# Kernel tuning notes

Hardware: AMD Instinct MI355X
Metric: run time of the kernel (lower is better)

## Reference

```python
import jax, jax.numpy as jnp
import numpy as np
import math

B, N, D = 4, 1024, 1024
H = 16
HD = D // H          # 64
TOP_K = 64
NUM_STATIC = 32


def setup_inputs() -> dict:
    key = jax.random.key(0)
    ks = jax.random.split(key, 10)
    s = 1.0 / math.sqrt(D)  # ~ nn.Linear default init scale
    inp = {
        "x": jax.random.normal(ks[0], (B, N, D), dtype=jnp.float32),
        "Wq": jax.random.uniform(ks[1], (D, D), jnp.float32, -s, s),
        "bq": jax.random.uniform(ks[2], (D,), jnp.float32, -s, s),
        "Wk": jax.random.uniform(ks[3], (D, D), jnp.float32, -s, s),
        "bk": jax.random.uniform(ks[4], (D,), jnp.float32, -s, s),
        "Wv": jax.random.uniform(ks[5], (D, D), jnp.float32, -s, s),
        "bv": jax.random.uniform(ks[6], (D,), jnp.float32, -s, s),
        "Wo": jax.random.uniform(ks[7], (D, D), jnp.float32, -s, s),
        "bo": jax.random.uniform(ks[8], (D,), jnp.float32, -s, s),
        "static_keys": jax.random.normal(ks[9], (NUM_STATIC, D), dtype=jnp.float32),
    }
    return inp


def _heads(t):
    # [B, N, D] -> [B, H, N, HD]
    return t.reshape(B, N, H, HD).transpose(0, 2, 1, 3)


def reference(x, Wq, bq, Wk, bk, Wv, bv, Wo, bo, static_keys):
    Q = _heads(x @ Wq.T + bq)
    K = _heads(x @ Wk.T + bk)
    V = _heads(x @ Wv.T + bv)

    # Replace the first NUM_STATIC key slots with learned static keys.
    K_stat = static_keys.reshape(1, NUM_STATIC, H, HD).transpose(0, 2, 1, 3)  # [1,H,S,HD]
    K_stat = jnp.broadcast_to(K_stat, (B, H, NUM_STATIC, HD))
    K = jnp.concatenate([K_stat, K[:, :, NUM_STATIC:, :]], axis=2)  # [B,H,N,HD]

    scores = jnp.einsum("bhnd,bhmd->bhnm", Q, K) / math.sqrt(HD)  # [B,H,N,N]

    # top-k mask: keep top_k scores per query, -inf elsewhere
    top_scores, top_idx = jax.lax.top_k(scores, TOP_K)  # [B,H,N,K]
    bi = jnp.arange(B)[:, None, None, None]
    hi = jnp.arange(H)[None, :, None, None]
    ni = jnp.arange(N)[None, None, :, None]
    masked = jnp.full(scores.shape, -jnp.inf, dtype=scores.dtype)
    masked = masked.at[bi, hi, ni, top_idx].set(top_scores)

    attn = jax.nn.softmax(masked, axis=-1)
    out = jnp.einsum("bhnm,bhmd->bhnd", attn, V)  # [B,H,N,HD]
    out = out.transpose(0, 2, 1, 3).reshape(B, N, D)
    return out @ Wo.T + bo
```

## Files before the change

### kernel.cpp

```cpp
#include <hip/hip_runtime.h>

#define NSTAT 32
#define MAXSEL 76

typedef __attribute__((ext_vector_type(8))) short bf16x8_t;
typedef __attribute__((ext_vector_type(4))) float f32x4_t;

#define GLOAD_LDS16(g, l) \
    __builtin_amdgcn_global_load_lds((const __attribute__((address_space(1))) void*)(g), \
                                     (__attribute__((address_space(3))) void*)(l), 16, 0, 0)

__device__ __forceinline__ ushort rtn_bf16(float a) {
    unsigned u = __float_as_uint(a);
    return (ushort)((u + 0x7FFFu + ((u >> 16) & 1u)) >> 16);
}
__device__ __forceinline__ void limb2(float a, ushort& h, ushort& l) {
    ushort hh = rtn_bf16(a);
    float fh = __uint_as_float(((unsigned)hh) << 16);
    float r1 = a - fh;
    l = rtn_bf16(r1);
    h = hh;
}

__global__ __launch_bounds__(256)
void decomp_w_kernel(const float* __restrict__ Wq, const float* __restrict__ Wk,
                     const float* __restrict__ Wv, const float* __restrict__ Wo,
                     ushort* __restrict__ WLq, ushort* __restrict__ WoLb)
{
    const int m = blockIdx.y;
    const float* src = (m == 0) ? Wq : (m == 1) ? Wk : (m == 2) ? Wv : Wo;
    const int idx = blockIdx.x * 256 + threadIdx.x;
    const int e8 = idx * 8;
    const int row = e8 >> 10, k0 = e8 & 1023;
    const int kt = k0 >> 5, q = (k0 >> 3) & 3;
    const size_t doff = ((size_t)row << 10) + (size_t)(kt * 32) + (size_t)((q ^ (row & 3)) * 8);

    float4 v0 = *(const float4*)(src + e8);
    float4 v1 = *(const float4*)(src + e8 + 4);
    float f[8] = {v0.x, v0.y, v0.z, v0.w, v1.x, v1.y, v1.z, v1.w};

    const size_t Mi = (size_t)1 << 20;
    ushort h[8], l[8];
    #pragma unroll
    for (int e = 0; e < 8; ++e) limb2(f[e], h[e], l[e]);
    ushort* H = (m == 3) ? WoLb : WLq + (size_t)(m * 2) * Mi;
    ushort* L = H + Mi;
    *(ushort4*)(H + doff)     = make_ushort4(h[0],h[1],h[2],h[3]);
    *(ushort4*)(H + doff + 4) = make_ushort4(h[4],h[5],h[6],h[7]);
    *(ushort4*)(L + doff)     = make_ushort4(l[0],l[1],l[2],l[3]);
    *(ushort4*)(L + doff + 4) = make_ushort4(l[4],l[5],l[6],l[7]);
}

__global__ __launch_bounds__(256, 3)
void limb_gemm_kernel(const float* __restrict__ A,
                      const ushort* __restrict__ WLq, const ushort* __restrict__ WoLb,
                      const float* __restrict__ bq, const float* __restrict__ bk,
                      const float* __restrict__ bv, const float* __restrict__ bo,
                      const float* __restrict__ statk,
                      float* __restrict__ Qw, float* __restrict__ Vw,
                      ushort* __restrict__ KHo, ushort* __restrict__ KLo,
                      float* __restrict__ Cout, int is_out)
{
    __shared__ __align__(16) ushort Al[2][128][32];
    __shared__ __align__(16) ushort Bl[2][2][128][32];

    const int t = threadIdx.x;
    const int bx = blockIdx.x, by = blockIdx.y;
    const int mode = is_out ? 3 : (int)blockIdx.z;
    const int wc0 = bx * 128;
    const int arow0 = by * 128;

    const size_t Mi = (size_t)1 << 20;
    const ushort* BpH;
    const float* bias;
    if (mode == 0)      { BpH = WLq;          bias = bq; }
    else if (mode == 1) { BpH = WLq + 2*Mi;   bias = bk; }
    else if (mode == 2) { BpH = WLq + 4*Mi;   bias = bv; }
    else                { BpH = WoLb;         bias = bo; }
    const ushort* BpL = BpH + Mi;

    const int ll = t & 63, w = t >> 6;

    f32x4_t acc[4][4];
    #pragma unroll
    for (int i = 0; i < 4; ++i)
        #pragma unroll
        for (int j = 0; j < 4; ++j) acc[i][j] = (f32x4_t){0.f, 0.f, 0.f, 0.f};

    auto stageB = [&](int kt, int bb) {
        #pragma unroll
        for (int limb = 0; limb < 2; ++limb) {
            const ushort* src = limb ? BpL : BpH;
            #pragma unroll
            for (int call = 0; call < 2; ++call) {
                int chunk = (w * 2 + call) * 64 + ll;
                int eoff = chunk * 8;
                int row = eoff >> 5, qp = (eoff >> 3) & 3;
                const ushort* g = src + ((size_t)(wc0 + row) << 10) + kt * 32 + qp * 8;
                char* l = ((char*)&Bl[bb][limb][0][0]) + (w * 2 + call) * 1024;
                GLOAD_LDS16(g, l);
            }
        }
    };
    const int srow = t >> 1, skh = (t & 1) * 16;
    auto loadA = [&](int kt, float4* a4) {
        const float* p = A + (((size_t)(arow0 + srow)) << 10) + kt * 32 + skh;
        a4[0] = *(const float4*)(p + 0);
        a4[1] = *(const float4*)(p + 4);
        a4[2] = *(const float4*)(p + 8);
        a4[3] = *(const float4*)(p + 12);
    };
    auto writeA = [&](const float4* a4) {
        float f[16];
        #pragma unroll
        for (int i = 0; i < 4; ++i) {
            f[i*4+0] = a4[i].x; f[i*4+1] = a4[i].y; f[i*4+2] = a4[i].z; f[i*4+3] = a4[i].w;
        }
        ushort h[16], lo[16];
        #pragma unroll
        for (int e = 0; e < 16; ++e) limb2(f[e], h[e], lo[e]);
        const int sw = srow & 3;
        #pragma unroll
        for (int qq = 0; qq < 2; ++qq) {
            int q = (skh >> 3) + qq;
            int qo = (q ^ sw) * 8;
            bf16x8_t vH, vL;
            #pragma unroll
            for (int e = 0; e < 8; ++e) {
                vH[e] = (short)h[qq*8+e]; vL[e] = (short)lo[qq*8+e];
            }
            *(bf16x8_t*)&Al[0][srow][qo] = vH;
            *(bf16x8_t*)&Al[1][srow][qo] = vL;
        }
    };

    const int wr = (w >> 1) * 64, wcv = (w & 1) * 64;
    const int fr = ll & 15, kg = ll >> 4;

    auto compute = [&](int bb) {
        bf16x8_t af[4][2];
        #pragma unroll
        for (int i = 0; i < 4; ++i) {
            int row = wr + i * 16 + fr;
            int qo = (kg ^ (row & 3)) * 8;
            af[i][0] = *(const bf16x8_t*)&Al[0][row][qo];
            af[i][1] = *(const bf16x8_t*)&Al[1][row][qo];
        }
        #pragma unroll
        for (int j = 0; j < 4; ++j) {
            int row = wcv + j * 16 + fr;
            int qo = (kg ^ (row & 3)) * 8;
            bf16x8_t b0 = *(const bf16x8_t*)&Bl[bb][0][row][qo];
            bf16x8_t b1 = *(const bf16x8_t*)&Bl[bb][1][row][qo];
            #pragma unroll
            for (int i = 0; i < 4; ++i) {
                acc[i][j] = __builtin_amdgcn_mfma_f32_16x16x32_bf16(af[i][0], b0, acc[i][j], 0, 0, 0);
                acc[i][j] = __builtin_amdgcn_mfma_f32_16x16x32_bf16(af[i][0], b1, acc[i][j], 0, 0, 0);
                acc[i][j] = __builtin_amdgcn_mfma_f32_16x16x32_bf16(af[i][1], b0, acc[i][j], 0, 0, 0);
            }
        }
    };

    float4 a4[4];
    loadA(0, a4);
    writeA(a4);
    stageB(0, 0);
    __syncthreads();

    float4 a4n[4];
    for (int kt = 0; kt < 32; ++kt) {
        int bb = kt & 1;
        if (kt < 31) {
            stageB(kt + 1, bb ^ 1);
            loadA(kt + 1, a4n);
        }
        compute(bb);
        __syncthreads();
        if (kt < 31) writeA(a4n);
        __syncthreads();
    }

    #pragma unroll
    for (int i = 0; i < 4; ++i) {
        #pragma unroll
        for (int j = 0; j < 4; ++j) {
            int c = wc0 + wcv + j * 16 + (ll & 15);
            float bv_ = bias[c];
            #pragma unroll
            for (int q = 0; q < 4; ++q) {
                int gr = arow0 + wr + i * 16 + (kg) * 4 + q;
                float v = acc[i][j][q] + bv_;
                if (mode == 3) {
                    Cout[(size_t)gr * 1024 + c] = v;
                } else {
                    int b = gr >> 10, n = gr & 1023;
                    int h = c >> 6, d = c & 63;
                    size_t bhn = ((size_t)(b * 16 + h)) * 1024 + n;
                    if (mode == 1) {
                        if (n < NSTAT) v = statk[n * 1024 + c];
                        ushort kh, klo;
                        limb2(v, kh, klo);
                        size_t off = bhn * 64 + (size_t)(((d >> 3) ^ (n & 7)) * 8) + (d & 7);
                        KHo[off] = kh;
                        KLo[off] = klo;
                    } else {
                        float* Out = (mode == 0) ? Qw : Vw;
                        Out[bhn * 64 + d] = v;
                    }
                }
            }
        }
    }
}

__device__ __forceinline__ void radix_stage7(int* __restrict__ hist, int r, int l,
                                             const unsigned* __restrict__ ku,
                                             unsigned pref, unsigned mask, int shift,
                                             int tgt, int2* __restrict__ piv)
{
    #pragma unroll
    for (int b = 0; b < 8; ++b) hist[(l*8 + b)*33 + r] = 0;
    __syncthreads();
    #pragma unroll
    for (int j = 0; j < 64; ++j) {
        unsigned k = ku[j];
        if ((k & mask) == pref)
            atomicAdd(&hist[(int)((k >> shift) & 127u)*33 + r], 1);
    }
    __syncthreads();
    int seg = 0;
    #pragma unroll
    for (int b = 0; b < 8; ++b) seg += hist[(l*8 + b)*33 + r];
    int suf = seg;
    #pragma unroll
    for (int off = 1; off < 16; off <<= 1) {
        int v = __shfl_down(suf, off, 16);
        suf += (l + off < 16) ? v : 0;
    }
    const int above = suf - seg;
    if (above < tgt && above + seg >= tgt) {
        int c = above;
        #pragma unroll
        for (int b = 7; b >= 0; --b) {
            int h = hist[(l*8 + b)*33 + r];
            if (c + h >= tgt) { piv[r] = make_int2(l*8 + b, tgt - c); break; }
            c += h;
        }
    }
    __syncthreads();
}

__global__ __launch_bounds__(512, 4)
void attn_mfma_kernel(const float* __restrict__ Qw,
                      const ushort* __restrict__ KH, const ushort* __restrict__ KL,
                      const float* __restrict__ Vw, float* __restrict__ outp)
{
    __shared__ __align__(16) char pool[59904];
    __shared__ int2 piv[32];
    __shared__ int cnt[32];
    __shared__ float rowsum[32];

    int* hist = (int*)pool;
    float (*Qs)[68] = (float(*)[68])(pool + 32768);
    uint2 (*sel)[MAXSEL] = (uint2(*)[MAXSEL])pool;

    const int t = threadIdx.x;
    const int bid0 = blockIdx.x;
    const int bid = (bid0 & 7) * 256 + (bid0 >> 3);
    const int qt = bid & 31;
    const int bh = bid >> 5;
    const int n0 = qt * 32;
    const float* Qbase = Qw + ((size_t)bh * 1024 + n0) * 64;
    const float* Vbase = Vw + (size_t)bh * 1024 * 64;
    const ushort* KHb = KH + (size_t)bh * 1024 * 64;
    const ushort* KLb = KL + (size_t)bh * 1024 * 64;

    const int ll = t & 63;
    const int w  = t >> 6;
    const int qh = w >> 2;
    const int kr = w & 3;
    const int r  = t >> 4, l = t & 15;

    {
        int q = t >> 4, dq = (t & 15) * 4;
        *(float4*)&Qs[q][dq] = *(const float4*)(Qbase + q * 64 + dq);
    }
    auto stageK = [&](int c, int kb) {
        const ushort* gH = KHb + (size_t)c * 4096 + t * 8;
        const ushort* gL = KLb + (size_t)c * 4096 + t * 8;
        char* dH = pool + kb * 16384 + t * 16;
        char* dL = pool + kb * 16384 + 8192 + t * 16;
        GLOAD_LDS16(gH, dH);
        GLOAD_LDS16(gL, dL);
    };
    stageK(0, 0);
    if (t < 32) cnt[t] = 0;
    __syncthreads();

    bf16x8_t aH[2], aL[2];
    {
        const int arow = qh * 16 + (ll & 15), akg = ll >> 4;
        #pragma unroll
        for (int s = 0; s < 2; ++s) {
            const float* qp = &Qs[arow][s*32 + akg*8];
            float4 q0 = *(const float4*)qp;
            float4 q1 = *(const float4*)(qp + 4);
            float qv[8] = {q0.x,q0.y,q0.z,q0.w,q1.x,q1.y,q1.z,q1.w};
            #pragma unroll
            for (int j = 0; j < 8; ++j) {
                ushort hh, lo2;
                limb2(qv[j], hh, lo2);
                aH[s][j] = (short)hh; aL[s][j] = (short)lo2;
            }
        }
    }

    unsigned ku[64];

    #pragma unroll
    for (int c = 0; c < 16; ++c) {
        const int kb = c & 1;
        float (*scb)[72] = (float(*)[72])(pool + 41472 + kb * 9216);
        if (c < 15) stageK(c + 1, kb ^ 1);

        {
            const ushort* KH_l = (const ushort*)(pool + kb * 16384);
            const ushort* KL_l = KH_l + 4096;
            const int brow = kr * 16 + (ll & 15);
            f32x4_t a_ = {0.f, 0.f, 0.f, 0.f};
            #pragma unroll
            for (int s = 0; s < 2; ++s) {
                int q2 = (s*4 + (ll >> 4)) ^ (brow & 7);
                int off = brow*64 + q2*8;
                bf16x8_t bH = *(const bf16x8_t*)&KH_l[off];
                bf16x8_t bL = *(const bf16x8_t*)&KL_l[off];
                a_ = __builtin_amdgcn_mfma_f32_16x16x32_bf16(aH[s], bH, a_, 0, 0, 0);
                a_ = __builtin_amdgcn_mfma_f32_16x16x32_bf16(aH[s], bL, a_, 0, 0, 0);
                a_ = __builtin_amdgcn_mfma_f32_16x16x32_bf16(aL[s], bH, a_, 0, 0, 0);
            }
            const int qr = qh * 16 + (ll >> 4) * 4;
            scb[qr+0][brow] = a_[0];
            scb[qr+1][brow] = a_[1];
            scb[qr+2][brow] = a_[2];
            scb[qr+3][brow] = a_[3];
        }
        __syncthreads();

        {
            float4 v4 = *(const float4*)&scb[r][l*4];
            float vv[4] = {v4.x, v4.y, v4.z, v4.w};
            #pragma unroll
            for (int e = 0; e < 4; ++e) {
                float vc = fminf(fmaxf(vv[e], -31.9f), 31.9f);
                ku[c*4 + e] = (unsigned)(int)fmaf(vc, 32768.f, 1048576.f);
            }
        }
    }

    int tgt = 64;
    radix_stage7(hist, r, l, ku, 0u, 0u, 14, tgt, piv);
    unsigned pref = (unsigned)piv[r].x << 14; tgt = piv[r].y;
    radix_stage7(hist, r, l, ku, pref, 0x1FC000u, 7, tgt, piv);
    pref |= (unsigned)piv[r].x << 7; tgt = piv[r].y;
    radix_stage7(hist, r, l, ku, pref, 0x1FFF80u, 0, tgt, piv);
    const unsigned thr = pref | (unsigned)piv[r].x;

    const unsigned bhi = thr + 2u;
    const unsigned blo = thr - 2u;
    #pragma unroll
    for (int j = 0; j < 64; ++j) {
        unsigned k = ku[j];
        if (k >= blo) {
            int slot = atomicAdd(&cnt[r], 1);
            if (slot < MAXSEL)
                sel[r][slot] = make_uint2((unsigned)((j >> 2)*64 + l*4 + (j & 3)), k);
        }
    }
    __syncthreads();

    {
        int cc = cnt[r]; cc = (cc < MAXSEL) ? cc : MAXSEL;
        int Dl = 0, ml = 0;
        for (int j = l; j < cc; j += 16) {
            unsigned k = sel[r][j].y;
            if (k > bhi) Dl++; else ml++;
        }
        #pragma unroll
        for (int off = 8; off; off >>= 1) {
            Dl += __shfl_xor(Dl, off, 16);
            ml += __shfl_xor(ml, off, 16);
        }
        const float frac = (float)(64 - Dl) / (float)ml;
        float ls = 0.f;
        for (int j = l; j < cc; j += 16) {
            uint2 p = sel[r][j];
            float wgt = __expf((float)(int)(p.y - thr) * 3.814697265625e-6f);
            if (p.y <= bhi) wgt *= frac;
            p.y = __float_as_uint(wgt);
            sel[r][j] = p;
            ls += wgt;
        }
        #pragma unroll
        for (int off = 8; off; off >>= 1) ls += __shfl_xor(ls, off, 16);
        if (l == 0) { rowsum[r] = ls; cnt[r] = cc; }
    }
    __syncthreads();

    {
        const int pr = t >> 4;
        const int d4 = (t & 15) * 4;
        const int bb = bh >> 4, hh = bh & 15;
        const int cc = cnt[pr];
        float4 a = make_float4(0.f, 0.f, 0.f, 0.f);
        int j = 0;
        for (; j + 1 < cc; j += 2) {
            uint2 p0 = sel[pr][j];
            uint2 p1 = sel[pr][j+1];
            float w0 = __uint_as_float(p0.y);
            float w1 = __uint_as_float(p1.y);
            float4 v0 = *(const float4*)(Vbase + (size_t)p0.x * 64 + d4);
            float4 v1 = *(const float4*)(Vbase + (size_t)p1.x * 64 + d4);
            a.x += w0 * v0.x + w1 * v1.x;
            a.y += w0 * v0.y + w1 * v1.y;
            a.z += w0 * v0.z + w1 * v1.z;
            a.w += w0 * v0.w + w1 * v1.w;
        }
        if (j < cc) {
            uint2 p = sel[pr][j];
            float wv = __uint_as_float(p.y);
            float4 v = *(const float4*)(Vbase + (size_t)p.x * 64 + d4);
            a.x += wv * v.x; a.y += wv * v.y; a.z += wv * v.z; a.w += wv * v.w;
        }
        float inv = 1.0f / rowsum[pr];
        a.x *= inv; a.y *= inv; a.z *= inv; a.w *= inv;
        *(float4*)(outp + ((size_t)bb * 1024 + (n0 + pr)) * 1024 + hh * 64 + d4) = a;
    }
}

extern "C" void kernel_launch(void* const* d_in, const int* in_sizes, int n_in,
                              void* d_out, int out_size, void* d_ws, size_t ws_size,
                              hipStream_t stream) {
    const float* x     = (const float*)d_in[0];
    const float* Wq    = (const float*)d_in[1];
    const float* bq    = (const float*)d_in[2];
    const float* Wk    = (const float*)d_in[3];
    const float* bk    = (const float*)d_in[4];
    const float* Wv    = (const float*)d_in[5];
    const float* bv    = (const float*)d_in[6];
    const float* Wo    = (const float*)d_in[7];
    const float* bo    = (const float*)d_in[8];
    const float* statk = (const float*)d_in[9];
    float* out = (float*)d_out;
    char* base = (char*)d_ws;

    const size_t MiB = (size_t)1 << 20;
    float*  Qw   = (float*)(base);
    float*  Vw   = (float*)(base + 16*MiB);
    ushort* KH   = (ushort*)(base + 32*MiB);
    ushort* KL   = (ushort*)(base + 40*MiB);
    ushort* WoLb = (ushort*)(base + 48*MiB);
    ushort* WLq  = (ushort*)(base + 52*MiB);
    float*  op   = (float*)(base + 52*MiB);

    dim3 gd(512, 4);
    decomp_w_kernel<<<gd, 256, 0, stream>>>(Wq, Wk, Wv, Wo, WLq, WoLb);

    dim3 g1(8, 32, 3);
    limb_gemm_kernel<<<g1, 256, 0, stream>>>(x, WLq, WoLb, bq, bk, bv, bo, statk,
                                             Qw, Vw, KH, KL, nullptr, 0);

    attn_mfma_kernel<<<2048, 512, 0, stream>>>(Qw, KH, KL, Vw, op);

    dim3 g2(8, 32, 1);
    limb_gemm_kernel<<<g2, 256, 0, stream>>>(op, WLq, WoLb, bq, bk, bv, bo, statk,
                                             Qw, Vw, KH, KL, out, 1);
}
```

Measured before the change: 320.4 us.

## Pre-split x into bf16 limbs, specialize QKV GEMM, and widen attention key chunks

Adds a kernel that splits x once into bf16 hi/lo limbs in a swizzled layout, using the output buffer as scratch. A dedicated QKV GEMM then streams both A and B operands with direct global-to-LDS loads instead of converting fp32 A tiles in registers three times. This removes the repeated per-mode conversion of x and the register staging path, at the cost of an extra pass over x and lower occupancy (launch bounds 256,2). The attention kernel also processes 128-key chunks with a single K buffer and extra barriers instead of double-buffered 64-key chunks, trading load overlap for fewer iterations.

Result: no change. 319.7 us (-0.2%).

```diff
diff --git a/kernel.cpp b/kernel.cpp
--- a/kernel.cpp
+++ b/kernel.cpp
@@ -51,32 +51,160 @@
     *(ushort4*)(L + doff + 4) = make_ushort4(l[4],l[5],l[6],l[7]);
 }
 
+__global__ __launch_bounds__(256)
+void decomp_x_kernel(const float* __restrict__ x,
+                     ushort* __restrict__ XH, ushort* __restrict__ XL)
+{
+    const int idx = blockIdx.x * 256 + threadIdx.x;
+    const int e8 = idx * 8;
+    const int row = e8 >> 10, k0 = e8 & 1023;
+    const int kt = k0 >> 5, q = (k0 >> 3) & 3;
+    const size_t doff = ((size_t)row << 10) + (size_t)(kt * 32) + (size_t)((q ^ (row & 3)) * 8);
+
+    float4 v0 = *(const float4*)(x + e8);
+    float4 v1 = *(const float4*)(x + e8 + 4);
+    float f[8] = {v0.x, v0.y, v0.z, v0.w, v1.x, v1.y, v1.z, v1.w};
+    ushort h[8], l[8];
+    #pragma unroll
+    for (int e = 0; e < 8; ++e) limb2(f[e], h[e], l[e]);
+    *(ushort4*)(XH + doff)     = make_ushort4(h[0],h[1],h[2],h[3]);
+    *(ushort4*)(XH + doff + 4) = make_ushort4(h[4],h[5],h[6],h[7]);
+    *(ushort4*)(XL + doff)     = make_ushort4(l[0],l[1],l[2],l[3]);
+    *(ushort4*)(XL + doff + 4) = make_ushort4(l[4],l[5],l[6],l[7]);
+}
+
+__global__ __launch_bounds__(256, 2)
+void qkv_gemm_kernel(const ushort* __restrict__ XH, const ushort* __restrict__ XL,
+                     const ushort* __restrict__ WLq,
+                     const float* __restrict__ bq, const float* __restrict__ bk,
+                     const float* __restrict__ bv, const float* __restrict__ statk,
+                     float* __restrict__ Qw, float* __restrict__ Vw,
+                     ushort* __restrict__ KHo, ushort* __restrict__ KLo)
+{
+    __shared__ __align__(16) ushort Al[2][2][128][32];
+    __shared__ __align__(16) ushort Bl[2][2][128][32];
+
+    const int t = threadIdx.x;
+    const int bx = blockIdx.x, by = blockIdx.y;
+    const int mode = (int)blockIdx.z;
+    const int wc0 = bx * 128;
+    const int arow0 = by * 128;
+
+    const size_t Mi = (size_t)1 << 20;
+    const ushort* BpH = WLq + (size_t)(mode * 2) * Mi;
+    const ushort* BpL = BpH + Mi;
+    const float* bias = (mode == 0) ? bq : (mode == 1) ? bk : bv;
+
+    const int ll = t & 63, w = t >> 6;
+
+    f32x4_t acc[4][4];
+    #pragma unroll
+    for (int i = 0; i < 4; ++i)
+        #pragma unroll
+        for (int j = 0; j < 4; ++j) acc[i][j] = (f32x4_t){0.f, 0.f, 0.f, 0.f};
+
+    auto stageT = [&](const ushort* srcH, const ushort* srcL, int rowbase, int kt,
+                      ushort (*dst)[2][128][32], int bb) {
+        #pragma unroll
+        for (int limb = 0; limb < 2; ++limb) {
+            const ushort* src = limb ? srcL : srcH;
+            #pragma unroll
+            for (int call = 0; call < 2; ++call) {
+                int chunk = (w * 2 + call) * 64 + ll;
+                int eoff = chunk * 8;
+                int row = eoff >> 5, qp = (eoff >> 3) & 3;
+                const ushort* g = src + ((size_t)(rowbase + row) << 10) + kt * 32 + qp * 8;
+                char* l = ((char*)&dst[bb][limb][0][0]) + (w * 2 + call) * 1024;
+                GLOAD_LDS16(g, l);
+            }
+        }
+    };
+
+    const int wr = (w >> 1) * 64, wcv = (w & 1) * 64;
+    const int fr = ll & 15, kg = ll >> 4;
+
+    auto compute = [&](int bb) {
+        bf16x8_t af[4][2];
+        #pragma unroll
+        for (int i = 0; i < 4; ++i) {
+            int row = wr + i * 16 + fr;
+            int qo = (kg ^ (row & 3)) * 8;
+            af[i][0] = *(const bf16x8_t*)&Al[bb][0][row][qo];
+            af[i][1] = *(const bf16x8_t*)&Al[bb][1][row][qo];
+        }
+        #pragma unroll
+        for (int j = 0; j < 4; ++j) {
+            int row = wcv + j * 16 + fr;
+            int qo = (kg ^ (row & 3)) * 8;
+            bf16x8_t b0 = *(const bf16x8_t*)&Bl[bb][0][row][qo];
+            bf16x8_t b1 = *(const bf16x8_t*)&Bl[bb][1][row][qo];
+            #pragma unroll
+            for (int i = 0; i < 4; ++i) {
+                acc[i][j] = __builtin_amdgcn_mfma_f32_16x16x32_bf16(af[i][0], b0, acc[i][j], 0, 0, 0);
+                acc[i][j] = __builtin_amdgcn_mfma_f32_16x16x32_bf16(af[i][0], b1, acc[i][j], 0, 0, 0);
+                acc[i][j] = __builtin_amdgcn_mfma_f32_16x16x32_bf16(af[i][1], b0, acc[i][j], 0, 0, 0);
+            }
+        }
+    };
+
+    stageT(XH, XL, arow0, 0, Al, 0);
+    stageT(BpH, BpL, wc0, 0, Bl, 0);
+    __syncthreads();
+
+    for (int kt = 0; kt < 32; ++kt) {
+        int bb = kt & 1;
+        if (kt < 31) {
+            stageT(XH, XL, arow0, kt + 1, Al, bb ^ 1);
+            stageT(BpH, BpL, wc0, kt + 1, Bl, bb ^ 1);
+        }
+        compute(bb);
+        __syncthreads();
+    }
+
+    #pragma unroll
+    for (int i = 0; i < 4; ++i) {
+        #pragma unroll
+        for (int j = 0; j < 4; ++j) {
+            int c = wc0 + wcv + j * 16 + (ll & 15);
+            float bv_ = bias[c];
+            #pragma unroll
+            for (int q = 0; q < 4; ++q) {
+                int gr = arow0 + wr + i * 16 + kg * 4 + q;
+                float v = acc[i][j][q] + bv_;
+                int b = gr >> 10, n = gr & 1023;
+                int h = c >> 6, d = c & 63;
+                size_t bhn = ((size_t)(b * 16 + h)) * 1024 + n;
+                if (mode == 1) {
+                    if (n < NSTAT) v = statk[n * 1024 + c];
+                    ushort kh, klo;
+                    limb2(v, kh, klo);
+                    size_t off = bhn * 64 + (size_t)(((d >> 3) ^ (n & 7)) * 8) + (d & 7);
+                    KHo[off] = kh;
+                    KLo[off] = klo;
+                } else {
+                    float* Out = (mode == 0) ? Qw : Vw;
+                    Out[bhn * 64 + d] = v;
+                }
+            }
+        }
+    }
+}
+
 __global__ __launch_bounds__(256, 3)
-void limb_gemm_kernel(const float* __restrict__ A,
-                      const ushort* __restrict__ WLq, const ushort* __restrict__ WoLb,
-                      const float* __restrict__ bq, const float* __restrict__ bk,
-                      const float* __restrict__ bv, const float* __restrict__ bo,
-                      const float* __restrict__ statk,
-                      float* __restrict__ Qw, float* __restrict__ Vw,
-                      ushort* __restrict__ KHo, ushort* __restrict__ KLo,
-                      float* __restrict__ Cout, int is_out)
+void out_gemm_kernel(const float* __restrict__ A,
+                     const ushort* __restrict__ WoLb, const float* __restrict__ bo,
+                     float* __restrict__ Cout)
 {
     __shared__ __align__(16) ushort Al[2][128][32];
     __shared__ __align__(16) ushort Bl[2][2][128][32];
 
     const int t = threadIdx.x;
     const int bx = blockIdx.x, by = blockIdx.y;
-    const int mode = is_out ? 3 : (int)blockIdx.z;
     const int wc0 = bx * 128;
     const int arow0 = by * 128;
 
     const size_t Mi = (size_t)1 << 20;
-    const ushort* BpH;
-    const float* bias;
-    if (mode == 0)      { BpH = WLq;          bias = bq; }
-    else if (mode == 1) { BpH = WLq + 2*Mi;   bias = bk; }
-    else if (mode == 2) { BpH = WLq + 4*Mi;   bias = bv; }
-    else                { BpH = WoLb;         bias = bo; }
+    const ushort* BpH = WoLb;
     const ushort* BpL = BpH + Mi;
 
     const int ll = t & 63, w = t >> 6;
@@ -185,29 +313,11 @@
         #pragma unroll
         for (int j = 0; j < 4; ++j) {
             int c = wc0 + wcv + j * 16 + (ll & 15);
-            float bv_ = bias[c];
+            float bv_ = bo[c];
             #pragma unroll
             for (int q = 0; q < 4; ++q) {
-                int gr = arow0 + wr + i * 16 + (kg) * 4 + q;
-                float v = acc[i][j][q] + bv_;
-                if (mode == 3) {
-                    Cout[(size_t)gr * 1024 + c] = v;
-                } else {
-                    int b = gr >> 10, n = gr & 1023;
-                    int h = c >> 6, d = c & 63;
-                    size_t bhn = ((size_t)(b * 16 + h)) * 1024 + n;
-                    if (mode == 1) {
-                        if (n < NSTAT) v = statk[n * 1024 + c];
-                        ushort kh, klo;
-                        limb2(v, kh, klo);
-                        size_t off = bhn * 64 + (size_t)(((d >> 3) ^ (n & 7)) * 8) + (d & 7);
-                        KHo[off] = kh;
-                        KLo[off] = klo;
-                    } else {
-                        float* Out = (mode == 0) ? Qw : Vw;
-                        Out[bhn * 64 + d] = v;
-                    }
-                }
+                int gr = arow0 + wr + i * 16 + kg * 4 + q;
+                Cout[(size_t)gr * 1024 + c] = acc[i][j][q] + bv_;
             }
         }
     }
@@ -255,14 +365,17 @@
                       const ushort* __restrict__ KH, const ushort* __restrict__ KL,
                       const float* __restrict__ Vw, float* __restrict__ outp)
 {
-    __shared__ __align__(16) char pool[59904];
+    __shared__ __align__(16) char pool[58368];
     __shared__ int2 piv[32];
     __shared__ int cnt[32];
     __shared__ float rowsum[32];
 
+    ushort* Klds0 = (ushort*)pool;
+    ushort* Klds1 = Klds0 + 8192;
     int* hist = (int*)pool;
-    float (*Qs)[68] = (float(*)[68])(pool + 32768);
-    uint2 (*sel)[MAXSEL] = (uint2(*)[MAXSEL])pool;
+    float (*Qs)[68]  = (float(*)[68])(pool + 32768);
+    float (*sc)[132] = (float(*)[132])(pool + 41472);
+    uint2 (*sel)[MAXSEL] = (uint2(*)[MAXSEL])(pool + 32768);
 
     const int t = threadIdx.x;
     const int bid0 = blockIdx.x;
@@ -285,15 +398,16 @@
         int q = t >> 4, dq = (t & 15) * 4;
         *(float4*)&Qs[q][dq] = *(const float4*)(Qbase + q * 64 + dq);
     }
-    auto stageK = [&](int c, int kb) {
-        const ushort* gH = KHb + (size_t)c * 4096 + t * 8;
-        const ushort* gL = KLb + (size_t)c * 4096 + t * 8;
-        char* dH = pool + kb * 16384 + t * 16;
-        char* dL = pool + kb * 16384 + 8192 + t * 16;
-        GLOAD_LDS16(gH, dH);
-        GLOAD_LDS16(gL, dL);
-    };
-    stageK(0, 0);
+    auto stageK = [&](int c) {
+        const size_t cb = (size_t)c * 8192;
+        #pragma unroll
+        for (int i = 0; i < 2; ++i) {
+            int boff = i * 8192 + w * 1024;
+            GLOAD_LDS16(KHb + cb + boff / 2 + ll * 8, ((char*)Klds0) + boff);
+            GLOAD_LDS16(KLb + cb + boff / 2 + ll * 8, ((char*)Klds1) + boff);
+        }
+    };
+    stageK(0);
     if (t < 32) cnt[t] = 0;
     __syncthreads();
 
@@ -314,47 +428,48 @@
             }
         }
     }
+    __syncthreads();
 
     unsigned ku[64];
 
     #pragma unroll
-    for (int c = 0; c < 16; ++c) {
-        const int kb = c & 1;
-        float (*scb)[72] = (float(*)[72])(pool + 41472 + kb * 9216);
-        if (c < 15) stageK(c + 1, kb ^ 1);
-
-        {
-            const ushort* KH_l = (const ushort*)(pool + kb * 16384);
-            const ushort* KL_l = KH_l + 4096;
-            const int brow = kr * 16 + (ll & 15);
+    for (int c = 0; c < 8; ++c) {
+        #pragma unroll
+        for (int tile = 0; tile < 2; ++tile) {
+            const int m0 = kr * 32 + tile * 16;
+            const int brow = m0 + (ll & 15);
             f32x4_t a_ = {0.f, 0.f, 0.f, 0.f};
             #pragma unroll
             for (int s = 0; s < 2; ++s) {
                 int q2 = (s*4 + (ll >> 4)) ^ (brow & 7);
                 int off = brow*64 + q2*8;
-                bf16x8_t bH = *(const bf16x8_t*)&KH_l[off];
-                bf16x8_t bL = *(const bf16x8_t*)&KL_l[off];
+                bf16x8_t bH = *(const bf16x8_t*)&Klds0[off];
+                bf16x8_t bL = *(const bf16x8_t*)&Klds1[off];
                 a_ = __builtin_amdgcn_mfma_f32_16x16x32_bf16(aH[s], bH, a_, 0, 0, 0);
                 a_ = __builtin_amdgcn_mfma_f32_16x16x32_bf16(aH[s], bL, a_, 0, 0, 0);
                 a_ = __builtin_amdgcn_mfma_f32_16x16x32_bf16(aL[s], bH, a_, 0, 0, 0);
             }
             const int qr = qh * 16 + (ll >> 4) * 4;
-            scb[qr+0][brow] = a_[0];
-            scb[qr+1][brow] = a_[1];
-            scb[qr+2][brow] = a_[2];
-            scb[qr+3][brow] = a_[3];
+            const int mcol = m0 + (ll & 15);
+            sc[qr+0][mcol] = a_[0];
+            sc[qr+1][mcol] = a_[1];
+            sc[qr+2][mcol] = a_[2];
+            sc[qr+3][mcol] = a_[3];
         }
         __syncthreads();
 
+        if (c < 7) stageK(c + 1);
         {
-            float4 v4 = *(const float4*)&scb[r][l*4];
-            float vv[4] = {v4.x, v4.y, v4.z, v4.w};
-            #pragma unroll
-            for (int e = 0; e < 4; ++e) {
+            float4 v0 = *(const float4*)&sc[r][l*8];
+            float4 v1 = *(const float4*)&sc[r][l*8 + 4];
+            float vv[8] = {v0.x,v0.y,v0.z,v0.w,v1.x,v1.y,v1.z,v1.w};
+            #pragma unroll
+            for (int e = 0; e < 8; ++e) {
                 float vc = fminf(fmaxf(vv[e], -31.9f), 31.9f);
-                ku[c*4 + e] = (unsigned)(int)fmaf(vc, 32768.f, 1048576.f);
-            }
-        }
+                ku[c*8 + e] = (unsigned)(int)fmaf(vc, 32768.f, 1048576.f);
+            }
+        }
+        __syncthreads();
     }
 
     int tgt = 64;
@@ -373,7 +488,7 @@
         if (k >= blo) {
             int slot = atomicAdd(&cnt[r], 1);
             if (slot < MAXSEL)
-                sel[r][slot] = make_uint2((unsigned)((j >> 2)*64 + l*4 + (j & 3)), k);
+                sel[r][slot] = make_uint2((unsigned)((j >> 3)*128 + l*8 + (j & 7)), k);
         }
     }
     __syncthreads();
@@ -461,17 +576,19 @@
     ushort* WoLb = (ushort*)(base + 48*MiB);
     ushort* WLq  = (ushort*)(base + 52*MiB);
     float*  op   = (float*)(base + 52*MiB);
+    ushort* XH   = (ushort*)d_out;
+    ushort* XL   = XH + ((size_t)4 << 20);
 
     dim3 gd(512, 4);
     decomp_w_kernel<<<gd, 256, 0, stream>>>(Wq, Wk, Wv, Wo, WLq, WoLb);
+    decomp_x_kernel<<<2048, 256, 0, stream>>>(x, XH, XL);
 
     dim3 g1(8, 32, 3);
-    limb_gemm_kernel<<<g1, 256, 0, stream>>>(x, WLq, WoLb, bq, bk, bv, bo, statk,
-                                             Qw, Vw, KH, KL, nullptr, 0);
+    qkv_gemm_kernel<<<g1, 256, 0, stream>>>(XH, XL, WLq, bq, bk, bv, statk,
+                                            Qw, Vw, KH, KL);
 
     attn_mfma_kernel<<<2048, 512, 0, stream>>>(Qw, KH, KL, Vw, op);
 
-    dim3 g2(8, 32, 1);
-    limb_gemm_kernel<<<g2, 256, 0, stream>>>(op, WLq, WoLb, bq, bk, bv, bo, statk,
-                                             Qw, Vw, KH, KL, out, 1);
-}
+    dim3 g2(8, 32);
+    out_gemm_kernel<<<g2, 256, 0, stream>>>(op, WoLb, bo, out);
+}
```
